# Performance work log

Hardware: AMD Instinct MI355X
Metric: run time of the kernel (lower is better)

## Reference

```python
import jax, jax.numpy as jnp
import numpy as np

N = 50000   # nodes
E = 600000  # edges
D = 128     # in = hidden = out channels
L = 3       # num_layers
LN_EPS = 1e-5


def setup_inputs() -> dict:
    key = jax.random.key(0)
    ks = jax.random.split(key, 4)
    x = jax.random.normal(ks[0], (N, D), dtype=jnp.float32)
    edge_index = jax.random.randint(ks[1], (2, E), 0, N, dtype=jnp.int32)
    # GCNConv linear weights (glorot-ish scale) and biases, one per layer
    Ws = jax.random.normal(ks[2], (L, D, D), dtype=jnp.float32) / np.sqrt(D)
    bs = jnp.zeros((L, D), dtype=jnp.float32)
    # LayerNorm affine params per layer
    ln_w = jnp.ones((L, D), dtype=jnp.float32)
    ln_b = jnp.zeros((L, D), dtype=jnp.float32)
    # PReLU (single shared slope per layer, torch default init 0.25)
    alphas = jnp.full((L,), 0.25, dtype=jnp.float32)
    return {"x": x, "edge_index": edge_index, "Ws": Ws, "bs": bs,
            "ln_w": ln_w, "ln_b": ln_b, "alphas": alphas}


def reference(x, edge_index, Ws, bs, ln_w, ln_b, alphas):
    # --- gcn_norm: add self-loops, symmetric D^{-1/2} (A+I) D^{-1/2} ---
    loop = jnp.arange(N, dtype=edge_index.dtype)
    src = jnp.concatenate([edge_index[0], loop])  # [E+N]
    dst = jnp.concatenate([edge_index[1], loop])  # [E+N]
    deg = jax.ops.segment_sum(jnp.ones_like(dst, dtype=x.dtype), dst,
                              num_segments=N)
    dinv = jnp.where(deg > 0, jax.lax.rsqrt(jnp.maximum(deg, 1.0)), 0.0)
    norm = (dinv[src] * dinv[dst])[:, None]  # [E+N, 1]

    h = x
    for l in range(L):
        # GCNConv: linear -> gather -> scale -> scatter-add -> bias
        h = h @ Ws[l]                                   # [N, D]
        msg = h[src] * norm                             # [E+N, D]
        h = jax.ops.segment_sum(msg, dst, num_segments=N) + bs[l]
        # LayerNorm over feature dim
        mu = jnp.mean(h, axis=-1, keepdims=True)
        var = jnp.mean((h - mu) ** 2, axis=-1, keepdims=True)
        h = (h - mu) * jax.lax.rsqrt(var + LN_EPS) * ln_w[l] + ln_b[l]
        # PReLU
        h = jnp.where(h >= 0, h, alphas[l] * h)
    return h
```

## Files before the change

kernel.cpp:

```cpp
#include <hip/hip_runtime.h>
#include <hip/hip_bf16.h>

#define NN 50000
#define EE 600000
#define DD 128
#define LL 3
#define LN_EPS 1e-5f
#define CAP 64
#define ALD 136
#define POOL 16
#define G0BLK ((NN + 31) / 32)

typedef __attribute__((ext_vector_type(8))) short short8;
typedef __attribute__((ext_vector_type(4))) float floatx4;

__device__ inline unsigned short f2bf(float f) {
    union { float f; unsigned u; } a; a.f = f;
    unsigned r = a.u + 0x7fffu + ((a.u >> 16) & 1u);
    return (unsigned short)(r >> 16);
}


__global__ __launch_bounds__(256) void init_kernel(const float* __restrict__ W,
                                                   unsigned short* __restrict__ Wt,
                                                   int* __restrict__ cnt) {
    for (int i = blockIdx.x * 256 + threadIdx.x; i < NN; i += gridDim.x * 256)
        cnt[i] = 0;
    for (int i = blockIdx.x * 256 + threadIdx.x; i < LL * DD * DD; i += gridDim.x * 256) {
        int l = i >> 14, n = (i >> 7) & 127, k = i & 127;
        Wt[i] = f2bf(W[(l << 14) + k * DD + n]);
    }
}


__global__ __launch_bounds__(256) void gemm0_fill_kernel(
    const float* __restrict__ A, const unsigned short* __restrict__ Wt,
    const int* __restrict__ src, const int* __restrict__ dst,
    int* __restrict__ cnt, int* __restrict__ csrc,
    unsigned short* __restrict__ Cb) {
    __shared__ unsigned short alds[32 * ALD];
    int tid = threadIdx.x;

    for (int e = blockIdx.x * 256 + tid; e < EE; e += G0BLK * 256) {
        int d = dst[e];
        int pos = atomicAdd(&cnt[d], 1);
        csrc[(size_t)d * CAP + pos] = src[e];
    }

    int lane = tid & 63;
    int w = tid >> 6;
    int rowbase = blockIdx.x * 32;
    int cbase = (w & 1) * 64;
    int nIdx = cbase + (lane & 15);
    int kq = (lane >> 4) * 8;

    {
        int r = tid >> 3;
        int k0 = (tid & 7) * 16;
        int grow = rowbase + r;
        unsigned short* dstp = &alds[r * ALD + k0];
        if (grow < NN) {
            const float* ap = &A[(size_t)grow * DD + k0];
            float4 v0 = *(const float4*)&ap[0];
            float4 v1 = *(const float4*)&ap[4];
            float4 v2 = *(const float4*)&ap[8];
            float4 v3 = *(const float4*)&ap[12];
            float fv[16] = {v0.x,v0.y,v0.z,v0.w, v1.x,v1.y,v1.z,v1.w,
                            v2.x,v2.y,v2.z,v2.w, v3.x,v3.y,v3.z,v3.w};
            unsigned short uv[16];
            #pragma unroll
            for (int q = 0; q < 16; q++) uv[q] = f2bf(fv[q]);
            *(uint4*)&dstp[0] = *(uint4*)&uv[0];
            *(uint4*)&dstp[8] = *(uint4*)&uv[8];
        } else {
            uint4 z = make_uint4(0, 0, 0, 0);
            *(uint4*)&dstp[0] = z;
            *(uint4*)&dstp[8] = z;
        }
    }
    __syncthreads();

    int rbase = (w >> 1) * 16;
    int mrow = rbase + (lane & 15);
    floatx4 acc[4] = {{0.f,0.f,0.f,0.f},{0.f,0.f,0.f,0.f},
                      {0.f,0.f,0.f,0.f},{0.f,0.f,0.f,0.f}};
    #pragma unroll
    for (int t = 0; t < 4; t++) {
        short8 a = *(const short8*)&alds[mrow * ALD + t * 32 + kq];
        #pragma unroll
        for (int j = 0; j < 4; j++) {
            short8 b = *(const short8*)&Wt[(nIdx + j * 16) * DD + t * 32 + kq];
            acc[j] = __builtin_amdgcn_mfma_f32_16x16x32_bf16(a, b, acc[j], 0, 0, 0);
        }
    }

    int gnode0 = rowbase + rbase + (lane >> 4) * 4;
    #pragma unroll
    for (int i = 0; i < 4; i++) {
        int node = gnode0 + i;
        if (node < NN) {
            #pragma unroll
            for (int j = 0; j < 4; j++)
                Cb[(size_t)node * DD + cbase + j * 16 + (lane & 15)] = f2bf(acc[j][i]);
        }
    }
}


__device__ inline void acc_row_w(float* acc, uint4 t, float w) {
    unsigned uu[4] = {t.x, t.y, t.z, t.w};
    #pragma unroll
    for (int q = 0; q < 4; q++) {
        union { unsigned x; float f; } lo, hi;
        lo.x = uu[q] << 16;
        hi.x = uu[q] & 0xffff0000u;
        acc[2 * q]     += w * lo.f;
        acc[2 * q + 1] += w * hi.f;
    }
}

__device__ inline void agg_node(const unsigned short* __restrict__ Tb,
                                const int* __restrict__ cnt, const int* __restrict__ csrc,
                                const float* bv, const float* wv, const float* cv,
                                float alpha, int node, int f8, float* yv) {
    int deg = cnt[node];
    float dv = rsqrtf((float)(deg + 1));
    const int* row = &csrc[(size_t)node * CAP];

    float acc[8] = {};
    acc_row_w(acc, *(const uint4*)&Tb[(size_t)node * DD + f8], dv);

    int k = 0;
    for (; k + 4 <= deg; k += 4) {
        int4 ss = *(const int4*)&row[k];
        float w0 = rsqrtf((float)(cnt[ss.x] + 1));
        float w1 = rsqrtf((float)(cnt[ss.y] + 1));
        float w2 = rsqrtf((float)(cnt[ss.z] + 1));
        float w3 = rsqrtf((float)(cnt[ss.w] + 1));
        uint4 t0 = *(const uint4*)&Tb[(size_t)ss.x * DD + f8];
        uint4 t1 = *(const uint4*)&Tb[(size_t)ss.y * DD + f8];
        uint4 t2 = *(const uint4*)&Tb[(size_t)ss.z * DD + f8];
        uint4 t3 = *(const uint4*)&Tb[(size_t)ss.w * DD + f8];
        acc_row_w(acc, t0, w0); acc_row_w(acc, t1, w1);
        acc_row_w(acc, t2, w2); acc_row_w(acc, t3, w3);
    }
    for (; k < deg; k++) {
        int s = row[k];
        float w = rsqrtf((float)(cnt[s] + 1));
        acc_row_w(acc, *(const uint4*)&Tb[(size_t)s * DD + f8], w);
    }

    float a[8];
    float s1 = 0.f, s2 = 0.f;
    #pragma unroll
    for (int q = 0; q < 8; q++) {
        a[q] = fmaf(acc[q], dv, bv[q]);
        s1 += a[q]; s2 += a[q] * a[q];
    }
    #pragma unroll
    for (int off = 8; off > 0; off >>= 1) {
        s1 += __shfl_xor(s1, off, 16);
        s2 += __shfl_xor(s2, off, 16);
    }
    float mu = s1 * (1.f / DD);
    float var = s2 * (1.f / DD) - mu * mu;
    float rstd = rsqrtf(var + LN_EPS);
    #pragma unroll
    for (int q = 0; q < 8; q++) {
        float y = (a[q] - mu) * rstd * wv[q] + cv[q];
        yv[q] = (y >= 0.f) ? y : alpha * y;
    }
}


__global__ __launch_bounds__(256) void aggemm_kernel(
    const unsigned short* __restrict__ Tb, const int* __restrict__ cnt,
    const int* __restrict__ csrc,
    const float* __restrict__ bias, const float* __restrict__ lnw,
    const float* __restrict__ lnb, const float* __restrict__ alphas, int layer,
    const unsigned short* __restrict__ Wt, unsigned short* __restrict__ Tout) {
    __shared__ unsigned short alds[POOL * ALD];
    int tid = threadIdx.x;
    int g = tid >> 4;
    int lane16 = tid & 15;
    int f8 = lane16 * 8;
    int nodebase = blockIdx.x * POOL;

    float4 b0 = *(const float4*)&bias[f8];
    float4 b1 = *(const float4*)&bias[f8 + 4];
    float4 w0 = *(const float4*)&lnw[f8];
    float4 w1 = *(const float4*)&lnw[f8 + 4];
    float4 c0 = *(const float4*)&lnb[f8];
    float4 c1 = *(const float4*)&lnb[f8 + 4];
    float bv[8] = {b0.x, b0.y, b0.z, b0.w, b1.x, b1.y, b1.z, b1.w};
    float wv[8] = {w0.x, w0.y, w0.z, w0.w, w1.x, w1.y, w1.z, w1.w};
    float cv[8] = {c0.x, c0.y, c0.z, c0.w, c1.x, c1.y, c1.z, c1.w};
    float alpha = alphas[layer];

    {
        int node = nodebase + g;
        float yv[8];
        agg_node(Tb, cnt, csrc, bv, wv, cv, alpha, node, f8, yv);
        unsigned short pv[8];
        #pragma unroll
        for (int q = 0; q < 8; q++) pv[q] = f2bf(yv[q]);
        *(uint4*)&alds[g * ALD + f8] = *(uint4*)&pv[0];
    }
    __syncthreads();

    int lane = tid & 63;
    int w = tid >> 6;
    int cbase = w * 32;
    int kq = (lane >> 4) * 8;
    int mrow = lane & 15;
    floatx4 acc[2] = {{0.f,0.f,0.f,0.f},{0.f,0.f,0.f,0.f}};
    #pragma unroll
    for (int t = 0; t < 4; t++) {
        short8 a = *(const short8*)&alds[mrow * ALD + t * 32 + kq];
        #pragma unroll
        for (int j = 0; j < 2; j++) {
            short8 b = *(const short8*)&Wt[(cbase + j * 16 + (lane & 15)) * DD + t * 32 + kq];
            acc[j] = __builtin_amdgcn_mfma_f32_16x16x32_bf16(a, b, acc[j], 0, 0, 0);
        }
    }
    int gnode0 = nodebase + (lane >> 4) * 4;
    #pragma unroll
    for (int i = 0; i < 4; i++) {
        int node = gnode0 + i;
        #pragma unroll
        for (int j = 0; j < 2; j++)
            Tout[(size_t)node * DD + cbase + j * 16 + (lane & 15)] = f2bf(acc[j][i]);
    }
}


__global__ __launch_bounds__(256) void agg_final_kernel(
    const unsigned short* __restrict__ Tb, const int* __restrict__ cnt,
    const int* __restrict__ csrc,
    const float* __restrict__ bias, const float* __restrict__ lnw,
    const float* __restrict__ lnb, const float* __restrict__ alphas, int layer,
    float* __restrict__ out) {
    int g = threadIdx.x >> 4;
    int lane16 = threadIdx.x & 15;
    int f8 = lane16 * 8;
    int node = blockIdx.x * 16 + g;
    if (node >= NN) return;

    float4 b0 = *(const float4*)&bias[f8];
    float4 b1 = *(const float4*)&bias[f8 + 4];
    float4 w0 = *(const float4*)&lnw[f8];
    float4 w1 = *(const float4*)&lnw[f8 + 4];
    float4 c0 = *(const float4*)&lnb[f8];
    float4 c1 = *(const float4*)&lnb[f8 + 4];
    float bv[8] = {b0.x, b0.y, b0.z, b0.w, b1.x, b1.y, b1.z, b1.w};
    float wv[8] = {w0.x, w0.y, w0.z, w0.w, w1.x, w1.y, w1.z, w1.w};
    float cv[8] = {c0.x, c0.y, c0.z, c0.w, c1.x, c1.y, c1.z, c1.w};

    float yv[8];
    agg_node(Tb, cnt, csrc, bv, wv, cv, alphas[layer], node, f8, yv);

    float* op = &out[(size_t)node * DD + f8];
    *(float4*)&op[0] = make_float4(yv[0], yv[1], yv[2], yv[3]);
    *(float4*)&op[4] = make_float4(yv[4], yv[5], yv[6], yv[7]);
}


extern "C" void kernel_launch(void* const* d_in, const int* in_sizes, int n_in,
                              void* d_out, int out_size, void* d_ws, size_t ws_size,
                              hipStream_t stream) {
    const float* x    = (const float*)d_in[0];
    const int*   ei   = (const int*)d_in[1];
    const float* Ws   = (const float*)d_in[2];
    const float* bs   = (const float*)d_in[3];
    const float* lnw  = (const float*)d_in[4];
    const float* lnb  = (const float*)d_in[5];
    const float* alphas = (const float*)d_in[6];
    float* out = (float*)d_out;

    const int* src = ei;
    const int* dst = ei + EE;

    char* ws = (char*)d_ws;
    size_t off = 0;
    auto alloc = [&](size_t bytes) -> void* {
        void* p = ws + off;
        off = (off + bytes + 255) & ~(size_t)255;
        return p;
    };
    int* cnt  = (int*)alloc(NN * sizeof(int));
    int* csrc = (int*)alloc((size_t)NN * CAP * sizeof(int));
    unsigned short* wt    = (unsigned short*)alloc((size_t)LL * DD * DD * sizeof(unsigned short));
    unsigned short* tbufA = (unsigned short*)alloc((size_t)NN * DD * sizeof(unsigned short));
    unsigned short* tbufB = (unsigned short*)alloc((size_t)NN * DD * sizeof(unsigned short));

    init_kernel<<<256, 256, 0, stream>>>(Ws, wt, cnt);
    gemm0_fill_kernel<<<G0BLK, 256, 0, stream>>>(x, wt, src, dst, cnt, csrc, tbufA);

    const int agg_grid = NN / POOL;
    aggemm_kernel<<<agg_grid, 256, 0, stream>>>(tbufA, cnt, csrc,
                                                bs + 0 * DD, lnw + 0 * DD, lnb + 0 * DD,
                                                alphas, 0, wt + 1 * DD * DD, tbufB);
    aggemm_kernel<<<agg_grid, 256, 0, stream>>>(tbufB, cnt, csrc,
                                                bs + 1 * DD, lnw + 1 * DD, lnb + 1 * DD,
                                                alphas, 1, wt + 2 * DD * DD, tbufA);
    agg_final_kernel<<<(NN + 15) / 16, 256, 0, stream>>>(tbufA, cnt, csrc,
                                                         bs + 2 * DD, lnw + 2 * DD, lnb + 2 * DD,
                                                         alphas, 2, out);
}
```

Measured before the change: 235.8 us.

## Stage GEMM outputs through LDS for coalesced stores and retile gemm0 to 16 rows

The first GEMM kernel now processes 16 nodes per block with each wave covering 32 output columns, matching the aggregation kernels. Each block also handles exactly one 256-edge chunk of the CSR fill instead of a strided loop. In both GEMM kernels the MFMA results are written to shared memory and then stored to global memory as 16-byte coalesced rows, replacing scattered 2-byte stores. Bounds checks are dropped because 50000 divides evenly by 16; this costs extra barriers and a larger grid.

```diff
diff --git a/kernel.cpp b/kernel.cpp
--- a/kernel.cpp
+++ b/kernel.cpp
@@ -9,7 +9,7 @@
 #define CAP 64
 #define ALD 136
 #define POOL 16
-#define G0BLK ((NN + 31) / 32)
+#define NBLKS (NN / POOL)
 
 typedef __attribute__((ext_vector_type(8))) short short8;
 typedef __attribute__((ext_vector_type(4))) float floatx4;
@@ -38,71 +38,63 @@
     const int* __restrict__ src, const int* __restrict__ dst,
     int* __restrict__ cnt, int* __restrict__ csrc,
     unsigned short* __restrict__ Cb) {
-    __shared__ unsigned short alds[32 * ALD];
+    __shared__ unsigned short alds[POOL * ALD];
     int tid = threadIdx.x;
-
-    for (int e = blockIdx.x * 256 + tid; e < EE; e += G0BLK * 256) {
-        int d = dst[e];
-        int pos = atomicAdd(&cnt[d], 1);
-        csrc[(size_t)d * CAP + pos] = src[e];
-    }
-
     int lane = tid & 63;
     int w = tid >> 6;
-    int rowbase = blockIdx.x * 32;
-    int cbase = (w & 1) * 64;
-    int nIdx = cbase + (lane & 15);
+
+    {
+        int e = blockIdx.x * 256 + tid;
+        if (e < EE) {
+            int d = dst[e];
+            int pos = atomicAdd(&cnt[d], 1);
+            csrc[(size_t)d * CAP + pos] = src[e];
+        }
+    }
+
+    {
+        int row = tid >> 4;
+        int kc = (tid & 15) * 8;
+        const float* ap = &A[(size_t)(blockIdx.x * POOL + row) * DD + kc];
+        float4 v0 = *(const float4*)&ap[0];
+        float4 v1 = *(const float4*)&ap[4];
+        float fv[8] = {v0.x, v0.y, v0.z, v0.w, v1.x, v1.y, v1.z, v1.w};
+        unsigned short uv[8];
+        #pragma unroll
+        for (int q = 0; q < 8; q++) uv[q] = f2bf(fv[q]);
+        *(uint4*)&alds[row * ALD + kc] = *(uint4*)&uv[0];
+    }
+    __syncthreads();
+
+    int cbase = w * 32;
     int kq = (lane >> 4) * 8;
-
-    {
-        int r = tid >> 3;
-        int k0 = (tid & 7) * 16;
-        int grow = rowbase + r;
-        unsigned short* dstp = &alds[r * ALD + k0];
-        if (grow < NN) {
-            const float* ap = &A[(size_t)grow * DD + k0];
-            float4 v0 = *(const float4*)&ap[0];
-            float4 v1 = *(const float4*)&ap[4];
-            float4 v2 = *(const float4*)&ap[8];
-            float4 v3 = *(const float4*)&ap[12];
-            float fv[16] = {v0.x,v0.y,v0.z,v0.w, v1.x,v1.y,v1.z,v1.w,
-                            v2.x,v2.y,v2.z,v2.w, v3.x,v3.y,v3.z,v3.w};
-            unsigned short uv[16];
-            #pragma unroll
-            for (int q = 0; q < 16; q++) uv[q] = f2bf(fv[q]);
-            *(uint4*)&dstp[0] = *(uint4*)&uv[0];
-            *(uint4*)&dstp[8] = *(uint4*)&uv[8];
-        } else {
-            uint4 z = make_uint4(0, 0, 0, 0);
-            *(uint4*)&dstp[0] = z;
-            *(uint4*)&dstp[8] = z;
-        }
-    }
-    __syncthreads();
-
-    int rbase = (w >> 1) * 16;
-    int mrow = rbase + (lane & 15);
-    floatx4 acc[4] = {{0.f,0.f,0.f,0.f},{0.f,0.f,0.f,0.f},
-                      {0.f,0.f,0.f,0.f},{0.f,0.f,0.f,0.f}};
+    int mrow = lane & 15;
+    floatx4 acc[2] = {{0.f,0.f,0.f,0.f},{0.f,0.f,0.f,0.f}};
     #pragma unroll
     for (int t = 0; t < 4; t++) {
         short8 a = *(const short8*)&alds[mrow * ALD + t * 32 + kq];
         #pragma unroll
-        for (int j = 0; j < 4; j++) {
-            short8 b = *(const short8*)&Wt[(nIdx + j * 16) * DD + t * 32 + kq];
+        for (int j = 0; j < 2; j++) {
+            short8 b = *(const short8*)&Wt[(cbase + j * 16 + (lane & 15)) * DD + t * 32 + kq];
             acc[j] = __builtin_amdgcn_mfma_f32_16x16x32_bf16(a, b, acc[j], 0, 0, 0);
         }
     }
-
-    int gnode0 = rowbase + rbase + (lane >> 4) * 4;
-    #pragma unroll
-    for (int i = 0; i < 4; i++) {
-        int node = gnode0 + i;
-        if (node < NN) {
+    __syncthreads();
+
+    {
+        int r0 = (lane >> 4) * 4;
+        #pragma unroll
+        for (int i = 0; i < 4; i++)
             #pragma unroll
-            for (int j = 0; j < 4; j++)
-                Cb[(size_t)node * DD + cbase + j * 16 + (lane & 15)] = f2bf(acc[j][i]);
-        }
+            for (int j = 0; j < 2; j++)
+                alds[(r0 + i) * ALD + cbase + j * 16 + (lane & 15)] = f2bf(acc[j][i]);
+    }
+    __syncthreads();
+    {
+        int srow = tid >> 4;
+        int scol = (tid & 15) * 8;
+        *(uint4*)&Cb[(size_t)(blockIdx.x * POOL + srow) * DD + scol] =
+            *(uint4*)&alds[srow * ALD + scol];
     }
 }
 
@@ -223,13 +215,22 @@
             acc[j] = __builtin_amdgcn_mfma_f32_16x16x32_bf16(a, b, acc[j], 0, 0, 0);
         }
     }
-    int gnode0 = nodebase + (lane >> 4) * 4;
-    #pragma unroll
-    for (int i = 0; i < 4; i++) {
-        int node = gnode0 + i;
-        #pragma unroll
-        for (int j = 0; j < 2; j++)
-            Tout[(size_t)node * DD + cbase + j * 16 + (lane & 15)] = f2bf(acc[j][i]);
+    __syncthreads();
+
+    {
+        int r0 = (lane >> 4) * 4;
+        #pragma unroll
+        for (int i = 0; i < 4; i++)
+            #pragma unroll
+            for (int j = 0; j < 2; j++)
+                alds[(r0 + i) * ALD + cbase + j * 16 + (lane & 15)] = f2bf(acc[j][i]);
+    }
+    __syncthreads();
+    {
+        int srow = tid >> 4;
+        int scol = (tid & 15) * 8;
+        *(uint4*)&Tout[(size_t)(nodebase + srow) * DD + scol] =
+            *(uint4*)&alds[srow * ALD + scol];
     }
 }
 
@@ -244,7 +245,6 @@
     int lane16 = threadIdx.x & 15;
     int f8 = lane16 * 8;
     int node = blockIdx.x * 16 + g;
-    if (node >= NN) return;
 
     float4 b0 = *(const float4*)&bias[f8];
     float4 b1 = *(const float4*)&bias[f8 + 4];
@@ -294,16 +294,15 @@
     unsigned short* tbufB = (unsigned short*)alloc((size_t)NN * DD * sizeof(unsigned short));
 
     init_kernel<<<256, 256, 0, stream>>>(Ws, wt, cnt);
-    gemm0_fill_kernel<<<G0BLK, 256, 0, stream>>>(x, wt, src, dst, cnt, csrc, tbufA);
-
-    const int agg_grid = NN / POOL;
-    aggemm_kernel<<<agg_grid, 256, 0, stream>>>(tbufA, cnt, csrc,
-                                                bs + 0 * DD, lnw + 0 * DD, lnb + 0 * DD,
-                                                alphas, 0, wt + 1 * DD * DD, tbufB);
-    aggemm_kernel<<<agg_grid, 256, 0, stream>>>(tbufB, cnt, csrc,
-                                                bs + 1 * DD, lnw + 1 * DD, lnb + 1 * DD,
-                                                alphas, 1, wt + 2 * DD * DD, tbufA);
-    agg_final_kernel<<<(NN + 15) / 16, 256, 0, stream>>>(tbufA, cnt, csrc,
-                                                         bs + 2 * DD, lnw + 2 * DD, lnb + 2 * DD,
-                                                         alphas, 2, out);
-}
+    gemm0_fill_kernel<<<NBLKS, 256, 0, stream>>>(x, wt, src, dst, cnt, csrc, tbufA);
+
+    aggemm_kernel<<<NBLKS, 256, 0, stream>>>(tbufA, cnt, csrc,
+                                             bs + 0 * DD, lnw + 0 * DD, lnb + 0 * DD,
+                                             alphas, 0, wt + 1 * DD * DD, tbufB);
+    aggemm_kernel<<<NBLKS, 256, 0, stream>>>(tbufB, cnt, csrc,
+                                             bs + 1 * DD, lnw + 1 * DD, lnb + 1 * DD,
+                                             alphas, 1, wt + 2 * DD * DD, tbufA);
+    agg_final_kernel<<<NBLKS, 256, 0, stream>>>(tbufA, cnt, csrc,
+                                                bs + 2 * DD, lnw + 2 * DD, lnb + 2 * DD,
+                                                alphas, 2, out);
+}
```

Measured after the change: 231.3 us. Within noise of the previous version (-1.9%).
